# Kernel tuning notes

Hardware: AMD Instinct MI355X
Metric: run time of the kernel (lower is better)

Reference implementation:

```python
import jax, jax.numpy as jnp
import numpy as np

B, T, D = 16, 512, 384
MAX_LEN = 4096

def setup_inputs() -> dict:
    key = jax.random.key(0)
    k1, k2 = jax.random.split(key)
    encoder_out = jax.random.normal(k1, (B, T, D), dtype=jnp.float32)
    durations = jax.random.randint(k2, (B, T), 0, 8, dtype=jnp.int32)
    return {"encoder_out": encoder_out, "durations": durations, "max_len": MAX_LEN}

def _expand(encoder_out, durations, max_len):
    # Inclusive cumulative durations per sample: cum[b, t] = sum_{s<=t} dur[b, s]
    cum = jnp.cumsum(durations, axis=1)                     # [B, T]
    mel_lens = cum[:, -1]                                   # [B]
    pos = jnp.arange(max_len, dtype=cum.dtype)              # [L]
    # Output frame l belongs to the first token t with cum[t] > l.
    tok_idx = jax.vmap(lambda c: jnp.searchsorted(c, pos, side='right'))(cum)  # [B, L]
    tok_idx = jnp.clip(tok_idx, 0, durations.shape[1] - 1)
    expanded = jnp.take_along_axis(encoder_out, tok_idx[:, :, None], axis=1)   # [B, L, D]
    # Zero positions beyond each sample's total duration (matches zeros init + sequential fill).
    valid = pos[None, :] < jnp.minimum(mel_lens, max_len)[:, None]             # [B, L]
    expanded = jnp.where(valid[:, :, None], expanded, jnp.zeros((), expanded.dtype))
    return expanded, mel_lens

def reference(encoder_out, durations, max_len):
    return _expand(encoder_out, durations, max_len)
```

## Files before the change

### kernel.cpp

```cpp
#include <hip/hip_runtime.h>


#define LR_B       16
#define LR_T       512
#define LR_D4      96
#define LR_FRAMES  64
#define LR_THREADS 512
#define LR_WAVES   (LR_THREADS / 64)

typedef float f32x4 __attribute__((ext_vector_type(4)));

__global__ __launch_bounds__(LR_THREADS)
void lr_expand_kernel(const f32x4* __restrict__ enc,
                      const int*   __restrict__ dur,
                      float*       __restrict__ out,
                      int max_len) {
    const int b    = blockIdx.y;
    const int pos0 = blockIdx.x * LR_FRAMES;
    const int tid  = threadIdx.x;
    const int lane = tid & 63;
    const int wid  = tid >> 6;

    __shared__ int s_cum[LR_T];
    __shared__ int s_wsum[LR_WAVES];
    __shared__ int s_tok[LR_FRAMES];

    int v = dur[b * LR_T + tid];
#pragma unroll
    for (int off = 1; off < 64; off <<= 1) {
        int n = __shfl_up(v, off, 64);
        if (lane >= off) v += n;
    }
    if (lane == 63) s_wsum[wid] = v;
    __syncthreads();
    int woff = 0;
#pragma unroll
    for (int w = 0; w < LR_WAVES; ++w)
        woff += (w < wid) ? s_wsum[w] : 0;
    s_cum[tid] = v + woff;
    __syncthreads();

    const int mel_raw = s_cum[LR_T - 1];
    const int mel     = min(mel_raw, max_len);

    if (blockIdx.x == 0 && tid == 0) {
        out[(size_t)LR_B * max_len * (LR_D4 * 4) + b] = (float)mel_raw;
    }

    f32x4* out4 = (f32x4*)out;
    const size_t out_base = ((size_t)b * max_len + pos0) * LR_D4;
    const f32x4 zero4 = {0.f, 0.f, 0.f, 0.f};

    if (pos0 >= mel) {
#pragma unroll
        for (int it = 0; it < (LR_FRAMES * LR_D4) / LR_THREADS; ++it) {
            int j   = it * LR_THREADS + tid;
            int f   = j / LR_D4;
            int pos = pos0 + f;
            if (pos >= max_len) continue;
            __builtin_nontemporal_store(zero4, &out4[out_base + j]);
        }
        return;
    }

    if (tid < LR_FRAMES) {
        int pos = pos0 + tid;
        int lo = 0, hi = LR_T;
        while (lo < hi) {
            int mid = (lo + hi) >> 1;
            if (s_cum[mid] <= pos) lo = mid + 1; else hi = mid;
        }
        s_tok[tid] = min(lo, LR_T - 1);
    }
    __syncthreads();

#pragma unroll
    for (int it = 0; it < (LR_FRAMES * LR_D4) / LR_THREADS; ++it) {
        int j   = it * LR_THREADS + tid;
        int f   = j / LR_D4;
        int d4  = j - f * LR_D4;
        int pos = pos0 + f;
        if (pos >= max_len) continue;
        f32x4 val = zero4;
        if (pos < mel) {
            val = enc[(size_t)(b * LR_T + s_tok[f]) * LR_D4 + d4];
        }
        __builtin_nontemporal_store(val, &out4[out_base + j]);
    }
}

extern "C" void kernel_launch(void* const* d_in, const int* in_sizes, int n_in,
                              void* d_out, int out_size, void* d_ws, size_t ws_size,
                              hipStream_t stream) {
    const f32x4* enc = (const f32x4*)d_in[0];
    const int*   dur = (const int*)d_in[1];
    float*       out = (float*)d_out;

    const int max_len = (out_size - LR_B) / (LR_B * LR_D4 * 4);

    dim3 grid((max_len + LR_FRAMES - 1) / LR_FRAMES, LR_B);
    lr_expand_kernel<<<grid, LR_THREADS, 0, stream>>>(enc, dur, out, max_len);
}
```

Measured before the change: 127.7 us.

## Split expansion into token-index precompute kernel and lightweight copy kernel

Adds a per-sample kernel that computes the prefix sum and the token index for every output frame once, writing them to workspace. A second kernel with smaller blocks (16 frames, 256 threads) then only gathers rows and stores them, which removes the scan that every block of the old kernel repeated. The trade-off is an extra launch and a dependency between the two kernels, plus a token-index round trip through global memory. The first kernel runs only 16 blocks, so its binary searches over all 4096 frames are serialised on few CUs. The old single-kernel path is kept as a fallback when workspace is missing.

```diff
diff --git a/kernel.cpp b/kernel.cpp
--- a/kernel.cpp
+++ b/kernel.cpp
@@ -4,11 +4,98 @@
 #define LR_B       16
 #define LR_T       512
 #define LR_D4      96
-#define LR_FRAMES  64
 #define LR_THREADS 512
 #define LR_WAVES   (LR_THREADS / 64)
 
+#define K2_THREADS 256
+#define K2_FRAMES  16
+
 typedef float f32x4 __attribute__((ext_vector_type(4)));
+
+__global__ __launch_bounds__(LR_THREADS)
+void lr_tok_kernel(const int* __restrict__ dur,
+                   int*       __restrict__ tok,
+                   float*     __restrict__ out,
+                   int max_len) {
+    const int b    = blockIdx.x;
+    const int tid  = threadIdx.x;
+    const int lane = tid & 63;
+    const int wid  = tid >> 6;
+
+    __shared__ int s_cum[LR_T];
+    __shared__ int s_wsum[LR_WAVES];
+
+    int v = dur[b * LR_T + tid];
+#pragma unroll
+    for (int off = 1; off < 64; off <<= 1) {
+        int n = __shfl_up(v, off, 64);
+        if (lane >= off) v += n;
+    }
+    if (lane == 63) s_wsum[wid] = v;
+    __syncthreads();
+    int woff = 0;
+#pragma unroll
+    for (int w = 0; w < LR_WAVES; ++w)
+        woff += (w < wid) ? s_wsum[w] : 0;
+    s_cum[tid] = v + woff;
+    __syncthreads();
+
+    const int mel_raw = s_cum[LR_T - 1];
+    const int mel     = min(mel_raw, max_len);
+
+    if (tid == 0) {
+        out[(size_t)LR_B * max_len * (LR_D4 * 4) + b] = (float)mel_raw;
+    }
+
+    for (int pos = tid; pos < max_len; pos += LR_THREADS) {
+        int t = -1;
+        if (pos < mel) {
+            int lo = 0, hi = LR_T;
+            while (lo < hi) {
+                int mid = (lo + hi) >> 1;
+                if (s_cum[mid] <= pos) lo = mid + 1; else hi = mid;
+            }
+            t = min(lo, LR_T - 1);
+        }
+        tok[b * max_len + pos] = t;
+    }
+}
+
+__global__ __launch_bounds__(K2_THREADS)
+void lr_copy_kernel(const f32x4* __restrict__ enc,
+                    const int*   __restrict__ tok,
+                    float*       __restrict__ out,
+                    int max_len) {
+    const int b    = blockIdx.y;
+    const int pos0 = blockIdx.x * K2_FRAMES;
+    const int tid  = threadIdx.x;
+
+    __shared__ int s_tok[K2_FRAMES];
+    if (tid < K2_FRAMES) {
+        int pos = pos0 + tid;
+        s_tok[tid] = (pos < max_len) ? tok[b * max_len + pos] : -1;
+    }
+    __syncthreads();
+
+    f32x4* out4 = (f32x4*)out;
+    const size_t out_base = ((size_t)b * max_len + pos0) * LR_D4;
+    const f32x4 zero4 = {0.f, 0.f, 0.f, 0.f};
+
+#pragma unroll
+    for (int it = 0; it < (K2_FRAMES * LR_D4) / K2_THREADS; ++it) {
+        int j   = it * K2_THREADS + tid;
+        int f   = j / LR_D4;
+        int d4  = j - f * LR_D4;
+        int pos = pos0 + f;
+        if (pos >= max_len) continue;
+        int t = s_tok[f];
+        f32x4 val = zero4;
+        if (t >= 0) {
+            val = enc[(size_t)(b * LR_T + t) * LR_D4 + d4];
+        }
+        __builtin_nontemporal_store(val, &out4[out_base + j]);
+    }
+}
 
 __global__ __launch_bounds__(LR_THREADS)
 void lr_expand_kernel(const f32x4* __restrict__ enc,
@@ -16,14 +103,14 @@
                       float*       __restrict__ out,
                       int max_len) {
     const int b    = blockIdx.y;
-    const int pos0 = blockIdx.x * LR_FRAMES;
+    const int pos0 = blockIdx.x * 64;
     const int tid  = threadIdx.x;
     const int lane = tid & 63;
     const int wid  = tid >> 6;
 
     __shared__ int s_cum[LR_T];
     __shared__ int s_wsum[LR_WAVES];
-    __shared__ int s_tok[LR_FRAMES];
+    __shared__ int s_tok[64];
 
     int v = dur[b * LR_T + tid];
 #pragma unroll
@@ -53,7 +140,7 @@
 
     if (pos0 >= mel) {
 #pragma unroll
-        for (int it = 0; it < (LR_FRAMES * LR_D4) / LR_THREADS; ++it) {
+        for (int it = 0; it < (64 * LR_D4) / LR_THREADS; ++it) {
             int j   = it * LR_THREADS + tid;
             int f   = j / LR_D4;
             int pos = pos0 + f;
@@ -63,7 +150,7 @@
         return;
     }
 
-    if (tid < LR_FRAMES) {
+    if (tid < 64) {
         int pos = pos0 + tid;
         int lo = 0, hi = LR_T;
         while (lo < hi) {
@@ -75,7 +162,7 @@
     __syncthreads();
 
 #pragma unroll
-    for (int it = 0; it < (LR_FRAMES * LR_D4) / LR_THREADS; ++it) {
+    for (int it = 0; it < (64 * LR_D4) / LR_THREADS; ++it) {
         int j   = it * LR_THREADS + tid;
         int f   = j / LR_D4;
         int d4  = j - f * LR_D4;
@@ -98,6 +185,14 @@
 
     const int max_len = (out_size - LR_B) / (LR_B * LR_D4 * 4);
 
-    dim3 grid((max_len + LR_FRAMES - 1) / LR_FRAMES, LR_B);
-    lr_expand_kernel<<<grid, LR_THREADS, 0, stream>>>(enc, dur, out, max_len);
+    const size_t ws_need = (size_t)LR_B * max_len * sizeof(int);
+    if (d_ws != nullptr && ws_size >= ws_need) {
+        int* tok = (int*)d_ws;
+        lr_tok_kernel<<<LR_B, LR_THREADS, 0, stream>>>(dur, tok, out, max_len);
+        dim3 g2((max_len + K2_FRAMES - 1) / K2_FRAMES, LR_B);
+        lr_copy_kernel<<<g2, K2_THREADS, 0, stream>>>(enc, tok, out, max_len);
+    } else {
+        dim3 grid((max_len + 63) / 64, LR_B);
+        lr_expand_kernel<<<grid, LR_THREADS, 0, stream>>>(enc, dur, out, max_len);
+    }
 }
```

New measurement: 128.9 us, median of 2. About the same (+1.0%).
